# Optimization experiments

Hardware: AMD Instinct MI355X
Metric: run time of the kernel (lower is better)

The kernel has to match this reference:

```python
import jax, jax.numpy as jnp
import numpy as np

B, N, C, H = 2, 2048, 768, 12
DH = C // H
SCALE = DH ** (-0.5)


def setup_inputs() -> dict:
    key = jax.random.key(0)
    k1, k2, k3, k4 = jax.random.split(key, 4)
    x = jax.random.normal(k1, (B, N, 1, C), dtype=jnp.float32)
    mask = jax.random.randint(k2, (B, N), 0, 2) > 0  # bool keep-mask
    w_qkv = jax.random.normal(k3, (3 * C, C), dtype=jnp.float32) * (C ** -0.5)
    w_proj = jax.random.normal(k4, (C, C), dtype=jnp.float32) * (C ** -0.5)
    b_proj = jnp.zeros((C,), dtype=jnp.float32)
    return {"x": x, "mask": mask, "w_qkv": w_qkv, "w_proj": w_proj, "b_proj": b_proj}


def reference(x, mask, w_qkv, w_proj, b_proj):
    Bs, N1, N2, Cs = x.shape  # N2 == 1 required by the original reshape
    # qkv: Linear(dim, 3*dim, bias=False) -> reshape (B,N1,3,H,Dh) -> (3,B,H,N1,Dh)
    qkv = jnp.einsum('bnoc,dc->bnod', x, w_qkv)  # (B,N1,1,3C)
    qkv = qkv.reshape(Bs, N1, 3, H, Cs // H).transpose(2, 0, 3, 1, 4)
    q, k, v = qkv[0], qkv[1], qkv[2]  # each (B,H,N,Dh)
    attn = jnp.einsum('bhid,bhjd->bhij', q, k) * SCALE  # (B,H,N,N)
    mask_value = -jnp.finfo(attn.dtype).max
    pair = mask[:, None, :] & mask[:, :, None]  # (B,N,N), broadcast over heads
    attn = jnp.where(pair[:, None, :, :], attn, mask_value)
    attn = jax.nn.softmax(attn, axis=-1)
    # dropout in eval mode -> identity
    out = jnp.einsum('bhij,bhjd->bhid', attn, v)  # (B,H,N,Dh)
    out = out.transpose(0, 2, 1, 3).reshape(Bs, N1, Cs)  # (B,N,C)
    out = out @ w_proj.T + b_proj
    return out
```

## Files before the change

kernel.cpp:

```cpp
#include <hip/hip_runtime.h>

#define NN 2048
#define CC 768
#define HH 12
#define SCALE2 0.18033688011112042f
#define NEGB  -3.0e35f

typedef __attribute__((ext_vector_type(4))) float f32x4;
typedef __attribute__((ext_vector_type(8))) short short8;
typedef __attribute__((ext_vector_type(8))) unsigned short u16x8;

#if __has_builtin(__builtin_amdgcn_exp2f)
#define EXP2(x) __builtin_amdgcn_exp2f(x)
#else
#define EXP2(x) exp2f(x)
#endif

static __device__ __forceinline__ unsigned short f2bf(float f) {
    unsigned u = __float_as_uint(f);
    u += 0x7FFFu + ((u >> 16) & 1u);
    return (unsigned short)(u >> 16);
}

static __device__ __forceinline__ f32x4 MFMA(u16x8 a, u16x8 b, f32x4 c) {
    union { u16x8 u; short8 s; } ua, ub;
    ua.u = a; ub.u = b;
    return __builtin_amdgcn_mfma_f32_16x16x32_bf16(ua.s, ub.s, c, 0, 0, 0);
}

static __device__ __forceinline__ void glds16(const void* g, void* l) {
    __builtin_amdgcn_global_load_lds(
        (const __attribute__((address_space(1))) unsigned int*)g,
        (__attribute__((address_space(3))) unsigned int*)l, 16, 0, 0);
}

__global__ void cvt_f32_bf16(const float* __restrict__ in,
                             unsigned short* __restrict__ out, int n8) {
    int i = blockIdx.x * blockDim.x + threadIdx.x;
    if (i >= n8) return;
    const f32x4* p = (const f32x4*)(in + (size_t)i * 8);
    f32x4 a = p[0], b = p[1];
    u16x8 o;
    o[0] = f2bf(a[0]); o[1] = f2bf(a[1]); o[2] = f2bf(a[2]); o[3] = f2bf(a[3]);
    o[4] = f2bf(b[0]); o[5] = f2bf(b[1]); o[6] = f2bf(b[2]); o[7] = f2bf(b[3]);
    *(u16x8*)(out + (size_t)i * 8) = o;
}

__launch_bounds__(256)
__global__ void gemm_bt(const unsigned short* __restrict__ A,
                        const unsigned short* __restrict__ Bt,
                        unsigned short* __restrict__ outB,
                        float* __restrict__ outF,
                        const float* __restrict__ bias,
                        int M, int N, int K, int qcols) {
    __shared__ __align__(16) unsigned short As[128][64];
    __shared__ __align__(16) unsigned short Bs[128][64];
    int tid = threadIdx.x, lane = tid & 63, w = tid >> 6;
    int wm = w >> 1, wn = w & 1;
    int li = lane & 15, g = lane >> 4;
    int bn = blockIdx.x, bm = blockIdx.y;

    f32x4 acc[4][4] = {};

    int lrow = lane >> 3, lsl = lane & 7;
    int xcol = (lsl ^ (lrow & 7)) * 8;
    const unsigned short* Ag = A  + (size_t)(bm * 128 + w * 32 + lrow) * K + xcol;
    const unsigned short* Bg = Bt + (size_t)(bn * 128 + w * 32 + lrow) * K + xcol;

    for (int k0 = 0; k0 < K; k0 += 64) {
        __syncthreads();
#pragma unroll
        for (int i = 0; i < 4; ++i) {
            glds16(Ag + (size_t)(i * 8) * K + k0, &As[w * 32 + i * 8][0]);
            glds16(Bg + (size_t)(i * 8) * K + k0, &Bs[w * 32 + i * 8][0]);
        }
        __syncthreads();
#pragma unroll
        for (int kk = 0; kk < 2; ++kk) {
            u16x8 af[4], bf[4];
#pragma unroll
            for (int mi = 0; mi < 4; ++mi)
                af[mi] = *(const u16x8*)&As[wm * 64 + mi * 16 + li][((4 * kk + g) ^ (li & 7)) * 8];
#pragma unroll
            for (int ni = 0; ni < 4; ++ni)
                bf[ni] = *(const u16x8*)&Bs[wn * 64 + ni * 16 + li][((4 * kk + g) ^ (li & 7)) * 8];
            __builtin_amdgcn_s_setprio(1);
#pragma unroll
            for (int mi = 0; mi < 4; ++mi)
#pragma unroll
                for (int ni = 0; ni < 4; ++ni)
                    acc[mi][ni] = MFMA(af[mi], bf[ni], acc[mi][ni]);
            __builtin_amdgcn_s_setprio(0);
        }
    }

#pragma unroll
    for (int mi = 0; mi < 4; ++mi) {
#pragma unroll
        for (int ni = 0; ni < 4; ++ni) {
#pragma unroll
            for (int r = 0; r < 4; ++r) {
                int row = bm * 128 + wm * 64 + mi * 16 + g * 4 + r;
                int col = bn * 128 + wn * 64 + ni * 16 + li;
                float v = acc[mi][ni][r];
                if (outB) {
                    if (col < qcols) v *= SCALE2;
                    outB[(size_t)row * N + col] = f2bf(v);
                } else {
                    outF[(size_t)row * N + col] = v + bias[col];
                }
            }
        }
    }
}

__launch_bounds__(256, 3)
__global__ void attn_kernel(const unsigned short* __restrict__ qkv,
                            const int* __restrict__ mask,
                            unsigned short* __restrict__ hout) {
    __shared__ __align__(16) unsigned short Ks[2][64][64];
    __shared__ __align__(16) unsigned int   Vp[2][64][32];
    __shared__ __align__(16) float pen[NN];

    int tid = threadIdx.x;
    int lane = tid & 63;
    int w = tid >> 6;
    int li = lane & 15, g = lane >> 4;

    int lb = (blockIdx.x & 7) * 96 + (blockIdx.x >> 3);
    int qb = lb & 31;
    int bh = lb >> 5;
    int b = bh / HH, head = bh % HH;
    const int* mb = mask + b * NN;

    {
        int i = tid * 8;
        union { int4 v; int a[4]; } m0, m1;
        m0.v = *(const int4*)&mb[i];
        m1.v = *(const int4*)&mb[i + 4];
        f32x4 p0, p1;
#pragma unroll
        for (int r = 0; r < 4; ++r) {
            p0[r] = m0.a[r] ? 0.f : NEGB;
            p1[r] = m1.a[r] ? 0.f : NEGB;
        }
        *(f32x4*)&pen[i] = p0;
        *(f32x4*)&pen[i + 4] = p1;
    }

    const unsigned short* qbase = qkv + (size_t)(b * NN) * 2304;

    int qrow = qb * 64 + w * 16 + li;
    const unsigned short* qp = qbase + (size_t)qrow * 2304 + head * 64;
    u16x8 qf0 = *(const u16x8*)(qp + g * 8);
    u16x8 qf1 = *(const u16x8*)(qp + 32 + g * 8);
    bool rk = mb[qrow] != 0;
    float pm = rk ? 1.0f : 0.0f;
    if (!rk) {
        qf0 = (u16x8)0;
        qf1 = (u16x8)0;
    }

    int xslot = ((lane & 7) ^ ((lane >> 3) & 7)) * 8;
    const unsigned short* kg = qbase + CC + head * 64 + xslot
                               + (size_t)(w * 16 + (lane >> 3)) * 2304;

    int vm = tid >> 3;
    int vkc = (tid & 7) * 8;
    int vcol = (vm & 16) | ((vm & 6) << 1) | ((vm & 8) >> 2) | (vm & 1);
    int vslot = vcol >> 2, vsub = vcol & 3;
    const unsigned short* vg = qbase + 2 * CC + head * 64 + vkc;

    u16x8 va, vb;
    auto stageK = [&](int buf, int kb) {
        glds16(kg + (size_t)kb * 2304,       &Ks[buf][w * 16][0]);
        glds16(kg + (size_t)(kb + 8) * 2304, &Ks[buf][w * 16 + 8][0]);
    };
    auto loadV = [&](int kb) {
        va = *(const u16x8*)(vg + (size_t)(kb + 2 * vm) * 2304);
        vb = *(const u16x8*)(vg + (size_t)(kb + 2 * vm + 1) * 2304);
    };
    auto writeV = [&](int buf) {
        union { u16x8 v; unsigned u[4]; } ua, ub;
        ua.v = va; ub.v = vb;
        unsigned* vp = &Vp[buf][0][0];
#pragma unroll
        for (int e = 0; e < 8; ++e) {
            int dd = (e + (tid & 7)) & 7;
            unsigned dw = __builtin_amdgcn_perm(ub.u[dd >> 1], ua.u[dd >> 1],
                                                (dd & 1) ? 0x07060302u : 0x05040100u);
            int d0 = vkc + dd;
            vp[d0 * 32 + ((vslot ^ (d0 & 7)) << 2) + vsub] = dw;
        }
    };

    stageK(0, 0);
    loadV(0);
    writeV(0);

    float m_st = -1e30f, l_st = 0.f;
    f32x4 acc[4] = {};
    int cur = 0;

    for (int kb = 0; kb < NN; kb += 64) {
        __syncthreads();
        int nx = cur ^ 1;
        bool more = (kb + 64 < NN);
        if (more) { stageK(nx, kb + 64); loadV(kb + 64); }

        f32x4 st[4];
        __builtin_amdgcn_s_setprio(1);
#pragma unroll
        for (int t = 0; t < 4; ++t) {
            const unsigned short* kr = &Ks[cur][t * 16 + li][0];
            u16x8 k0 = *(const u16x8*)(kr + ((g ^ (li & 7)) * 8));
            u16x8 k1 = *(const u16x8*)(kr + (((4 + g) ^ (li & 7)) * 8));
            f32x4 z = {};
            z = MFMA(k0, qf0, z);
            z = MFMA(k1, qf1, z);
            st[t] = z;
        }
        __builtin_amdgcn_s_setprio(0);

        const float* pp = &pen[kb];
        float tmax = -3.0e38f;
#pragma unroll
        for (int t = 0; t < 4; ++t) {
            f32x4 p4 = *(const f32x4*)&pp[t * 16 + g * 4];
            st[t] += p4 * pm;
            tmax = fmaxf(tmax, fmaxf(fmaxf(st[t][0], st[t][1]),
                                     fmaxf(st[t][2], st[t][3])));
        }
        tmax = fmaxf(tmax, __shfl_xor(tmax, 16));
        tmax = fmaxf(tmax, __shfl_xor(tmax, 32));
        if (__any(tmax > m_st)) {
            float mnew = fmaxf(m_st, tmax);
            float alpha = EXP2(m_st - mnew);
            float ar[4];
#pragma unroll
            for (int r = 0; r < 4; ++r) ar[r] = __shfl(alpha, g * 4 + r);
#pragma unroll
            for (int dt = 0; dt < 4; ++dt)
#pragma unroll
                for (int r = 0; r < 4; ++r) acc[dt][r] *= ar[r];
            l_st *= alpha;
            m_st = mnew;
        }
        float lsum = 0.f;
        union { unsigned u[8]; u16x8 v[2]; } pu;
#pragma unroll
        for (int t = 0; t < 4; ++t) {
            f32x4 e4;
#pragma unroll
            for (int r = 0; r < 4; ++r) { e4[r] = EXP2(st[t][r] - m_st); lsum += e4[r]; }
            pu.u[t * 2]     = __builtin_amdgcn_perm(__float_as_uint(e4[1]),
                                                    __float_as_uint(e4[0]), 0x07060302u);
            pu.u[t * 2 + 1] = __builtin_amdgcn_perm(__float_as_uint(e4[3]),
                                                    __float_as_uint(e4[2]), 0x07060302u);
        }
        lsum += __shfl_xor(lsum, 16);
        lsum += __shfl_xor(lsum, 32);
        l_st += lsum;

        __builtin_amdgcn_s_setprio(1);
#pragma unroll
        for (int h = 0; h < 2; ++h) {
#pragma unroll
            for (int dt = 0; dt < 4; ++dt) {
                const unsigned* vr = &Vp[cur][dt * 16 + li][0];
                u16x8 vf = *(const u16x8*)(vr + (((4 * h + g) ^ (li & 7)) << 2));
                acc[dt] = MFMA(pu.v[h], vf, acc[dt]);
            }
        }
        __builtin_amdgcn_s_setprio(0);

        if (more) writeV(nx);
        cur = nx;
    }

    float linv = 1.0f / l_st;
    float lr[4];
#pragma unroll
    for (int r = 0; r < 4; ++r) lr[r] = __shfl(linv, g * 4 + r);
    size_t obase = ((size_t)(b * NN + qb * 64 + w * 16)) * CC + head * 64;
#pragma unroll
    for (int dt = 0; dt < 4; ++dt) {
#pragma unroll
        for (int r = 0; r < 4; ++r) {
            hout[obase + (size_t)(g * 4 + r) * CC + dt * 16 + li] =
                f2bf(acc[dt][r] * lr[r]);
        }
    }
}

extern "C" void kernel_launch(void* const* d_in, const int* in_sizes, int n_in,
                              void* d_out, int out_size, void* d_ws, size_t ws_size,
                              hipStream_t stream) {
    const float* x     = (const float*)d_in[0];
    const int*   mask  = (const int*)d_in[1];
    const float* wqkv  = (const float*)d_in[2];
    const float* wproj = (const float*)d_in[3];
    const float* bproj = (const float*)d_in[4];
    float* out = (float*)d_out;

    unsigned short* x_bf     = (unsigned short*)d_ws;
    unsigned short* wqkv_bf  = x_bf + 3145728;
    unsigned short* wproj_bf = wqkv_bf + 1769472;
    unsigned short* qkv_bf   = wproj_bf + 589824;
    unsigned short* h_bf     = qkv_bf + 9437184;

    cvt_f32_bf16<<<1536, 256, 0, stream>>>(x, x_bf, 393216);
    cvt_f32_bf16<<<864, 256, 0, stream>>>(wqkv, wqkv_bf, 221184);
    cvt_f32_bf16<<<288, 256, 0, stream>>>(wproj, wproj_bf, 73728);

    gemm_bt<<<dim3(18, 32), 256, 0, stream>>>(x_bf, wqkv_bf, qkv_bf, nullptr,
                                              nullptr, 4096, 2304, 768, 768);
    attn_kernel<<<768, 256, 0, stream>>>(qkv_bf, mask, h_bf);
    gemm_bt<<<dim3(6, 32), 256, 0, stream>>>(h_bf, wproj_bf, nullptr, out,
                                             bproj, 4096, 768, 768, 0);
}
```

Measured before the change: 231.2 us.

## Process two query tiles per wave in attention, halve block threads

The attention kernel now runs 128 threads (2 waves) per block, and each wave handles 32 query rows as two 16-row tiles, so every K and V fragment read from LDS feeds two MFMAs. The V global load is issued two iterations ahead and written to LDS at the start of the next iteration, which deepens prefetch. A lazy rescale threshold (THR=12) skips the online-softmax max update unless the new max exceeds the running max by more than 12 in the log2 domain. These changes cut LDS traffic and rescale work per row, at the cost of higher register pressure and fewer waves per block to hide latency. The threshold also lets exp2 values grow up to 2^12 before bf16 packing, which could slightly affect accuracy.

```diff
diff --git a/kernel.cpp b/kernel.cpp
--- a/kernel.cpp
+++ b/kernel.cpp
@@ -5,6 +5,7 @@
 #define HH 12
 #define SCALE2 0.18033688011112042f
 #define NEGB  -3.0e35f
+#define THR   12.0f
 
 typedef __attribute__((ext_vector_type(4))) float f32x4;
 typedef __attribute__((ext_vector_type(8))) short short8;
@@ -114,7 +115,7 @@
     }
 }
 
-__launch_bounds__(256, 3)
+__launch_bounds__(128, 2)
 __global__ void attn_kernel(const unsigned short* __restrict__ qkv,
                             const int* __restrict__ mask,
                             unsigned short* __restrict__ hout) {
@@ -134,162 +135,183 @@
     const int* mb = mask + b * NN;
 
     {
-        int i = tid * 8;
-        union { int4 v; int a[4]; } m0, m1;
-        m0.v = *(const int4*)&mb[i];
-        m1.v = *(const int4*)&mb[i + 4];
-        f32x4 p0, p1;
-#pragma unroll
-        for (int r = 0; r < 4; ++r) {
-            p0[r] = m0.a[r] ? 0.f : NEGB;
-            p1[r] = m1.a[r] ? 0.f : NEGB;
-        }
-        *(f32x4*)&pen[i] = p0;
-        *(f32x4*)&pen[i + 4] = p1;
+        int i = tid * 16;
+#pragma unroll
+        for (int s = 0; s < 4; ++s) {
+            union { int4 v; int a[4]; } m4;
+            m4.v = *(const int4*)&mb[i + s * 4];
+            f32x4 p;
+#pragma unroll
+            for (int r = 0; r < 4; ++r) p[r] = m4.a[r] ? 0.f : NEGB;
+            *(f32x4*)&pen[i + s * 4] = p;
+        }
     }
 
     const unsigned short* qbase = qkv + (size_t)(b * NN) * 2304;
 
-    int qrow = qb * 64 + w * 16 + li;
-    const unsigned short* qp = qbase + (size_t)qrow * 2304 + head * 64;
-    u16x8 qf0 = *(const u16x8*)(qp + g * 8);
-    u16x8 qf1 = *(const u16x8*)(qp + 32 + g * 8);
-    bool rk = mb[qrow] != 0;
-    float pm = rk ? 1.0f : 0.0f;
-    if (!rk) {
-        qf0 = (u16x8)0;
-        qf1 = (u16x8)0;
+    u16x8 qf[2][2];
+    float pm[2];
+#pragma unroll
+    for (int qt = 0; qt < 2; ++qt) {
+        int qrow = qb * 64 + w * 32 + qt * 16 + li;
+        const unsigned short* qp = qbase + (size_t)qrow * 2304 + head * 64;
+        u16x8 a0 = *(const u16x8*)(qp + g * 8);
+        u16x8 a1 = *(const u16x8*)(qp + 32 + g * 8);
+        bool rk = mb[qrow] != 0;
+        pm[qt] = rk ? 1.f : 0.f;
+        if (!rk) { a0 = (u16x8)0; a1 = (u16x8)0; }
+        qf[qt][0] = a0; qf[qt][1] = a1;
     }
 
     int xslot = ((lane & 7) ^ ((lane >> 3) & 7)) * 8;
     const unsigned short* kg = qbase + CC + head * 64 + xslot
-                               + (size_t)(w * 16 + (lane >> 3)) * 2304;
-
-    int vm = tid >> 3;
+                               + (size_t)(w * 32 + (lane >> 3)) * 2304;
+
+    int m2 = tid >> 3;
     int vkc = (tid & 7) * 8;
-    int vcol = (vm & 16) | ((vm & 6) << 1) | ((vm & 8) >> 2) | (vm & 1);
-    int vslot = vcol >> 2, vsub = vcol & 3;
+    int ma = m2 * 2, mbp = ma + 1;
+    int vca = (ma & 16) | ((ma & 6) << 1) | ((ma & 8) >> 2) | (ma & 1);
+    int vcb = (mbp & 16) | ((mbp & 6) << 1) | ((mbp & 8) >> 2) | (mbp & 1);
     const unsigned short* vg = qbase + 2 * CC + head * 64 + vkc;
 
-    u16x8 va, vb;
+    u16x8 vr0, vr1, vr2, vr3;
     auto stageK = [&](int buf, int kb) {
-        glds16(kg + (size_t)kb * 2304,       &Ks[buf][w * 16][0]);
-        glds16(kg + (size_t)(kb + 8) * 2304, &Ks[buf][w * 16 + 8][0]);
+#pragma unroll
+        for (int s = 0; s < 4; ++s)
+            glds16(kg + (size_t)(kb + s * 8) * 2304, &Ks[buf][w * 32 + s * 8][0]);
     };
     auto loadV = [&](int kb) {
-        va = *(const u16x8*)(vg + (size_t)(kb + 2 * vm) * 2304);
-        vb = *(const u16x8*)(vg + (size_t)(kb + 2 * vm + 1) * 2304);
+        vr0 = *(const u16x8*)(vg + (size_t)(kb + 4 * m2) * 2304);
+        vr1 = *(const u16x8*)(vg + (size_t)(kb + 4 * m2 + 1) * 2304);
+        vr2 = *(const u16x8*)(vg + (size_t)(kb + 4 * m2 + 2) * 2304);
+        vr3 = *(const u16x8*)(vg + (size_t)(kb + 4 * m2 + 3) * 2304);
     };
     auto writeV = [&](int buf) {
-        union { u16x8 v; unsigned u[4]; } ua, ub;
-        ua.v = va; ub.v = vb;
+        union { u16x8 v; unsigned u[4]; } a0, a1, a2, a3;
+        a0.v = vr0; a1.v = vr1; a2.v = vr2; a3.v = vr3;
         unsigned* vp = &Vp[buf][0][0];
 #pragma unroll
         for (int e = 0; e < 8; ++e) {
             int dd = (e + (tid & 7)) & 7;
-            unsigned dw = __builtin_amdgcn_perm(ub.u[dd >> 1], ua.u[dd >> 1],
-                                                (dd & 1) ? 0x07060302u : 0x05040100u);
             int d0 = vkc + dd;
-            vp[d0 * 32 + ((vslot ^ (d0 & 7)) << 2) + vsub] = dw;
+            unsigned dwa = __builtin_amdgcn_perm(a1.u[dd >> 1], a0.u[dd >> 1],
+                                                 (dd & 1) ? 0x07060302u : 0x05040100u);
+            unsigned dwb = __builtin_amdgcn_perm(a3.u[dd >> 1], a2.u[dd >> 1],
+                                                 (dd & 1) ? 0x07060302u : 0x05040100u);
+            vp[d0 * 32 + (((vca >> 2) ^ (d0 & 7)) << 2) + (vca & 3)] = dwa;
+            vp[d0 * 32 + (((vcb >> 2) ^ (d0 & 7)) << 2) + (vcb & 3)] = dwb;
         }
     };
 
     stageK(0, 0);
     loadV(0);
     writeV(0);
-
-    float m_st = -1e30f, l_st = 0.f;
-    f32x4 acc[4] = {};
-    int cur = 0;
-
-    for (int kb = 0; kb < NN; kb += 64) {
+    loadV(64);
+
+    float m_st[2] = {-1e30f, -1e30f};
+    float l_st[2] = {0.f, 0.f};
+    f32x4 acc[2][4] = {};
+
+    for (int it = 0; it < 32; ++it) {
         __syncthreads();
-        int nx = cur ^ 1;
-        bool more = (kb + 64 < NN);
-        if (more) { stageK(nx, kb + 64); loadV(kb + 64); }
-
-        f32x4 st[4];
+        int cur = it & 1, nx = cur ^ 1;
+        if (it < 31) { writeV(nx); stageK(nx, (it + 1) * 64); }
+        if (it < 30) loadV((it + 2) * 64);
+
+        f32x4 st[2][4];
         __builtin_amdgcn_s_setprio(1);
 #pragma unroll
         for (int t = 0; t < 4; ++t) {
             const unsigned short* kr = &Ks[cur][t * 16 + li][0];
             u16x8 k0 = *(const u16x8*)(kr + ((g ^ (li & 7)) * 8));
             u16x8 k1 = *(const u16x8*)(kr + (((4 + g) ^ (li & 7)) * 8));
-            f32x4 z = {};
-            z = MFMA(k0, qf0, z);
-            z = MFMA(k1, qf1, z);
-            st[t] = z;
+            f32x4 z0 = {}, z1 = {};
+            z0 = MFMA(k0, qf[0][0], z0);
+            z1 = MFMA(k0, qf[1][0], z1);
+            z0 = MFMA(k1, qf[0][1], z0);
+            z1 = MFMA(k1, qf[1][1], z1);
+            st[0][t] = z0; st[1][t] = z1;
         }
         __builtin_amdgcn_s_setprio(0);
 
-        const float* pp = &pen[kb];
-        float tmax = -3.0e38f;
-#pragma unroll
-        for (int t = 0; t < 4; ++t) {
-            f32x4 p4 = *(const f32x4*)&pp[t * 16 + g * 4];
-            st[t] += p4 * pm;
-            tmax = fmaxf(tmax, fmaxf(fmaxf(st[t][0], st[t][1]),
-                                     fmaxf(st[t][2], st[t][3])));
-        }
-        tmax = fmaxf(tmax, __shfl_xor(tmax, 16));
-        tmax = fmaxf(tmax, __shfl_xor(tmax, 32));
-        if (__any(tmax > m_st)) {
-            float mnew = fmaxf(m_st, tmax);
-            float alpha = EXP2(m_st - mnew);
-            float ar[4];
-#pragma unroll
-            for (int r = 0; r < 4; ++r) ar[r] = __shfl(alpha, g * 4 + r);
-#pragma unroll
-            for (int dt = 0; dt < 4; ++dt)
-#pragma unroll
-                for (int r = 0; r < 4; ++r) acc[dt][r] *= ar[r];
-            l_st *= alpha;
-            m_st = mnew;
-        }
-        float lsum = 0.f;
-        union { unsigned u[8]; u16x8 v[2]; } pu;
-#pragma unroll
-        for (int t = 0; t < 4; ++t) {
-            f32x4 e4;
-#pragma unroll
-            for (int r = 0; r < 4; ++r) { e4[r] = EXP2(st[t][r] - m_st); lsum += e4[r]; }
-            pu.u[t * 2]     = __builtin_amdgcn_perm(__float_as_uint(e4[1]),
-                                                    __float_as_uint(e4[0]), 0x07060302u);
-            pu.u[t * 2 + 1] = __builtin_amdgcn_perm(__float_as_uint(e4[3]),
-                                                    __float_as_uint(e4[2]), 0x07060302u);
-        }
-        lsum += __shfl_xor(lsum, 16);
-        lsum += __shfl_xor(lsum, 32);
-        l_st += lsum;
+        const float* pp = &pen[it * 64];
+        f32x4 p4[4];
+#pragma unroll
+        for (int t = 0; t < 4; ++t) p4[t] = *(const f32x4*)&pp[t * 16 + g * 4];
+        float lmax[2] = {-3e38f, -3e38f};
+#pragma unroll
+        for (int qt = 0; qt < 2; ++qt)
+#pragma unroll
+            for (int t = 0; t < 4; ++t) {
+                st[qt][t] += p4[t] * pm[qt];
+                lmax[qt] = fmaxf(lmax[qt], fmaxf(fmaxf(st[qt][t][0], st[qt][t][1]),
+                                                 fmaxf(st[qt][t][2], st[qt][t][3])));
+            }
+        bool trig = (lmax[0] > m_st[0] + THR) || (lmax[1] > m_st[1] + THR);
+        if (__any(trig)) {
+#pragma unroll
+            for (int qt = 0; qt < 2; ++qt) {
+                float tm = lmax[qt];
+                tm = fmaxf(tm, __shfl_xor(tm, 16));
+                tm = fmaxf(tm, __shfl_xor(tm, 32));
+                float mnew = fmaxf(m_st[qt], tm);
+                float alpha = EXP2(m_st[qt] - mnew);
+                float ar[4];
+#pragma unroll
+                for (int r = 0; r < 4; ++r) ar[r] = __shfl(alpha, g * 4 + r);
+#pragma unroll
+                for (int dt = 0; dt < 4; ++dt)
+#pragma unroll
+                    for (int r = 0; r < 4; ++r) acc[qt][dt][r] *= ar[r];
+                l_st[qt] *= alpha;
+                m_st[qt] = mnew;
+            }
+        }
+        union { unsigned u[8]; u16x8 v[2]; } pu[2];
+#pragma unroll
+        for (int qt = 0; qt < 2; ++qt) {
+            float lsum = 0.f;
+#pragma unroll
+            for (int t = 0; t < 4; ++t) {
+                f32x4 e4;
+#pragma unroll
+                for (int r = 0; r < 4; ++r) { e4[r] = EXP2(st[qt][t][r] - m_st[qt]); lsum += e4[r]; }
+                pu[qt].u[t * 2]     = __builtin_amdgcn_perm(__float_as_uint(e4[1]),
+                                                            __float_as_uint(e4[0]), 0x07060302u);
+                pu[qt].u[t * 2 + 1] = __builtin_amdgcn_perm(__float_as_uint(e4[3]),
+                                                            __float_as_uint(e4[2]), 0x07060302u);
+            }
+            lsum += __shfl_xor(lsum, 16);
+            lsum += __shfl_xor(lsum, 32);
+            l_st[qt] += lsum;
+        }
 
         __builtin_amdgcn_s_setprio(1);
 #pragma unroll
-        for (int h = 0; h < 2; ++h) {
+        for (int h = 0; h < 2; ++h)
 #pragma unroll
             for (int dt = 0; dt < 4; ++dt) {
                 const unsigned* vr = &Vp[cur][dt * 16 + li][0];
                 u16x8 vf = *(const u16x8*)(vr + (((4 * h + g) ^ (li & 7)) << 2));
-                acc[dt] = MFMA(pu.v[h], vf, acc[dt]);
-            }
-        }
+                acc[0][dt] = MFMA(pu[0].v[h], vf, acc[0][dt]);
+                acc[1][dt] = MFMA(pu[1].v[h], vf, acc[1][dt]);
+            }
         __builtin_amdgcn_s_setprio(0);
-
-        if (more) writeV(nx);
-        cur = nx;
-    }
-
-    float linv = 1.0f / l_st;
-    float lr[4];
-#pragma unroll
-    for (int r = 0; r < 4; ++r) lr[r] = __shfl(linv, g * 4 + r);
-    size_t obase = ((size_t)(b * NN + qb * 64 + w * 16)) * CC + head * 64;
-#pragma unroll
-    for (int dt = 0; dt < 4; ++dt) {
-#pragma unroll
-        for (int r = 0; r < 4; ++r) {
-            hout[obase + (size_t)(g * 4 + r) * CC + dt * 16 + li] =
-                f2bf(acc[dt][r] * lr[r]);
-        }
+    }
+
+#pragma unroll
+    for (int qt = 0; qt < 2; ++qt) {
+        float linv = 1.0f / l_st[qt];
+        float lr[4];
+#pragma unroll
+        for (int r = 0; r < 4; ++r) lr[r] = __shfl(linv, g * 4 + r);
+        size_t obase = ((size_t)(b * NN + qb * 64 + w * 32 + qt * 16)) * CC + head * 64;
+#pragma unroll
+        for (int dt = 0; dt < 4; ++dt)
+#pragma unroll
+            for (int r = 0; r < 4; ++r)
+                hout[obase + (size_t)(g * 4 + r) * CC + dt * 16 + li] =
+                    f2bf(acc[qt][dt][r] * lr[r]);
     }
 }
 
@@ -315,7 +337,7 @@
 
     gemm_bt<<<dim3(18, 32), 256, 0, stream>>>(x_bf, wqkv_bf, qkv_bf, nullptr,
                                               nullptr, 4096, 2304, 768, 768);
-    attn_kernel<<<768, 256, 0, stream>>>(qkv_bf, mask, h_bf);
+    attn_kernel<<<768, 128, 0, stream>>>(qkv_bf, mask, h_bf);
     gemm_bt<<<dim3(6, 32), 256, 0, stream>>>(h_bf, wproj_bf, nullptr, out,
                                              bproj, 4096, 768, 768, 0);
 }
```

Measured after the change: 238.9 us. 1.03x slower.

## Load K directly to registers, widen KV tile to 128, lazy softmax rescale

Applied to the files above, without the earlier changes.

The attention kernel stops staging K through LDS and has each lane read its K fragments straight from global memory into registers. The KV tile per iteration grows from 64 to 128, with V double-buffered in LDS and prefetched two tiles ahead. The online-softmax rescale now fires only when the new max exceeds the running max by a threshold, skipping most rescales. The aim is fewer barriers and less LDS traffic per key, at the cost of uncoalesced, redundant K global loads, more register pressure, and larger exp2 arguments before the max catches up.

```diff
diff --git a/kernel.cpp b/kernel.cpp
--- a/kernel.cpp
+++ b/kernel.cpp
@@ -5,6 +5,7 @@
 #define HH 12
 #define SCALE2 0.18033688011112042f
 #define NEGB  -3.0e35f
+#define THR   12.0f
 
 typedef __attribute__((ext_vector_type(4))) float f32x4;
 typedef __attribute__((ext_vector_type(8))) short short8;
@@ -118,8 +119,7 @@
 __global__ void attn_kernel(const unsigned short* __restrict__ qkv,
                             const int* __restrict__ mask,
                             unsigned short* __restrict__ hout) {
-    __shared__ __align__(16) unsigned short Ks[2][64][64];
-    __shared__ __align__(16) unsigned int   Vp[2][64][32];
+    __shared__ __align__(16) unsigned int Vp[2][2][64][32];
     __shared__ __align__(16) float pen[NN];
 
     int tid = threadIdx.x;
@@ -155,86 +155,91 @@
     u16x8 qf0 = *(const u16x8*)(qp + g * 8);
     u16x8 qf1 = *(const u16x8*)(qp + 32 + g * 8);
     bool rk = mb[qrow] != 0;
-    float pm = rk ? 1.0f : 0.0f;
-    if (!rk) {
-        qf0 = (u16x8)0;
-        qf1 = (u16x8)0;
-    }
-
-    int xslot = ((lane & 7) ^ ((lane >> 3) & 7)) * 8;
-    const unsigned short* kg = qbase + CC + head * 64 + xslot
-                               + (size_t)(w * 16 + (lane >> 3)) * 2304;
-
-    int vm = tid >> 3;
+    float pm = rk ? 1.f : 0.f;
+    if (!rk) { qf0 = (u16x8)0; qf1 = (u16x8)0; }
+
+    const unsigned short* kp = qbase + CC + head * 64 + (size_t)li * 2304 + g * 8;
+
+    int a4 = tid >> 3;
     int vkc = (tid & 7) * 8;
-    int vcol = (vm & 16) | ((vm & 6) << 1) | ((vm & 8) >> 2) | (vm & 1);
-    int vslot = vcol >> 2, vsub = vcol & 3;
+    int sub = a4 >> 4;
+    int jp0 = (2 * a4) & 31, jp1 = jp0 + 1;
+    int vca = (jp0 & 16) | ((jp0 & 6) << 1) | ((jp0 & 8) >> 2) | (jp0 & 1);
+    int vcb = (jp1 & 16) | ((jp1 & 6) << 1) | ((jp1 & 8) >> 2) | (jp1 & 1);
     const unsigned short* vg = qbase + 2 * CC + head * 64 + vkc;
 
-    u16x8 va, vb;
-    auto stageK = [&](int buf, int kb) {
-        glds16(kg + (size_t)kb * 2304,       &Ks[buf][w * 16][0]);
-        glds16(kg + (size_t)(kb + 8) * 2304, &Ks[buf][w * 16 + 8][0]);
-    };
+    u16x8 vr0, vr1, vr2, vr3;
     auto loadV = [&](int kb) {
-        va = *(const u16x8*)(vg + (size_t)(kb + 2 * vm) * 2304);
-        vb = *(const u16x8*)(vg + (size_t)(kb + 2 * vm + 1) * 2304);
+        const unsigned short* p = vg + (size_t)(kb + 4 * a4) * 2304;
+        vr0 = *(const u16x8*)(p);
+        vr1 = *(const u16x8*)(p + 2304);
+        vr2 = *(const u16x8*)(p + 2 * 2304);
+        vr3 = *(const u16x8*)(p + 3 * 2304);
     };
     auto writeV = [&](int buf) {
-        union { u16x8 v; unsigned u[4]; } ua, ub;
-        ua.v = va; ub.v = vb;
-        unsigned* vp = &Vp[buf][0][0];
+        union { u16x8 v; unsigned u[4]; } a0, a1, a2, a3;
+        a0.v = vr0; a1.v = vr1; a2.v = vr2; a3.v = vr3;
+        unsigned* vp = &Vp[buf][sub][0][0];
 #pragma unroll
         for (int e = 0; e < 8; ++e) {
             int dd = (e + (tid & 7)) & 7;
-            unsigned dw = __builtin_amdgcn_perm(ub.u[dd >> 1], ua.u[dd >> 1],
-                                                (dd & 1) ? 0x07060302u : 0x05040100u);
             int d0 = vkc + dd;
-            vp[d0 * 32 + ((vslot ^ (d0 & 7)) << 2) + vsub] = dw;
+            unsigned dwa = __builtin_amdgcn_perm(a1.u[dd >> 1], a0.u[dd >> 1],
+                                                 (dd & 1) ? 0x07060302u : 0x05040100u);
+            unsigned dwb = __builtin_amdgcn_perm(a3.u[dd >> 1], a2.u[dd >> 1],
+                                                 (dd & 1) ? 0x07060302u : 0x05040100u);
+            vp[d0 * 32 + (((vca >> 2) ^ (d0 & 7)) << 2) + (vca & 3)] = dwa;
+            vp[d0 * 32 + (((vcb >> 2) ^ (d0 & 7)) << 2) + (vcb & 3)] = dwb;
         }
     };
 
-    stageK(0, 0);
     loadV(0);
     writeV(0);
+    loadV(128);
 
     float m_st = -1e30f, l_st = 0.f;
     f32x4 acc[4] = {};
-    int cur = 0;
-
-    for (int kb = 0; kb < NN; kb += 64) {
+
+    for (int it = 0; it < 16; ++it) {
         __syncthreads();
-        int nx = cur ^ 1;
-        bool more = (kb + 64 < NN);
-        if (more) { stageK(nx, kb + 64); loadV(kb + 64); }
-
-        f32x4 st[4];
+        int cur = it & 1, nx = cur ^ 1;
+        int kb = it * 128;
+        if (it < 15) writeV(nx);
+        if (it < 14) loadV(kb + 256);
+
+        u16x8 kf[8][2];
+#pragma unroll
+        for (int t = 0; t < 8; ++t) {
+            const unsigned short* kr = kp + (size_t)(kb + t * 16) * 2304;
+            kf[t][0] = *(const u16x8*)(kr);
+            kf[t][1] = *(const u16x8*)(kr + 32);
+        }
+
+        f32x4 st[8];
         __builtin_amdgcn_s_setprio(1);
 #pragma unroll
-        for (int t = 0; t < 4; ++t) {
-            const unsigned short* kr = &Ks[cur][t * 16 + li][0];
-            u16x8 k0 = *(const u16x8*)(kr + ((g ^ (li & 7)) * 8));
-            u16x8 k1 = *(const u16x8*)(kr + (((4 + g) ^ (li & 7)) * 8));
+        for (int t = 0; t < 8; ++t) {
             f32x4 z = {};
-            z = MFMA(k0, qf0, z);
-            z = MFMA(k1, qf1, z);
+            z = MFMA(kf[t][0], qf0, z);
+            z = MFMA(kf[t][1], qf1, z);
             st[t] = z;
         }
         __builtin_amdgcn_s_setprio(0);
 
         const float* pp = &pen[kb];
-        float tmax = -3.0e38f;
-#pragma unroll
-        for (int t = 0; t < 4; ++t) {
+        float lmax = -3e38f;
+#pragma unroll
+        for (int t = 0; t < 8; ++t) {
             f32x4 p4 = *(const f32x4*)&pp[t * 16 + g * 4];
             st[t] += p4 * pm;
-            tmax = fmaxf(tmax, fmaxf(fmaxf(st[t][0], st[t][1]),
+            lmax = fmaxf(lmax, fmaxf(fmaxf(st[t][0], st[t][1]),
                                      fmaxf(st[t][2], st[t][3])));
         }
-        tmax = fmaxf(tmax, __shfl_xor(tmax, 16));
-        tmax = fmaxf(tmax, __shfl_xor(tmax, 32));
-        if (__any(tmax > m_st)) {
-            float mnew = fmaxf(m_st, tmax);
+        if (__any(lmax > m_st + THR)) {
+            float tm = lmax;
+            tm = fmaxf(tm, __shfl_xor(tm, 16));
+            tm = fmaxf(tm, __shfl_xor(tm, 32));
+            float mnew = fmaxf(m_st, tm);
             float alpha = EXP2(m_st - mnew);
             float ar[4];
 #pragma unroll
@@ -247,35 +252,38 @@
             m_st = mnew;
         }
         float lsum = 0.f;
-        union { unsigned u[8]; u16x8 v[2]; } pu;
-#pragma unroll
-        for (int t = 0; t < 4; ++t) {
-            f32x4 e4;
-#pragma unroll
-            for (int r = 0; r < 4; ++r) { e4[r] = EXP2(st[t][r] - m_st); lsum += e4[r]; }
-            pu.u[t * 2]     = __builtin_amdgcn_perm(__float_as_uint(e4[1]),
-                                                    __float_as_uint(e4[0]), 0x07060302u);
-            pu.u[t * 2 + 1] = __builtin_amdgcn_perm(__float_as_uint(e4[3]),
-                                                    __float_as_uint(e4[2]), 0x07060302u);
-        }
+        union { unsigned u[8]; u16x8 v[2]; } pu[2];
+#pragma unroll
+        for (int s = 0; s < 2; ++s)
+#pragma unroll
+            for (int t = 0; t < 4; ++t) {
+                f32x4 e4;
+#pragma unroll
+                for (int r = 0; r < 4; ++r) {
+                    e4[r] = EXP2(st[s * 4 + t][r] - m_st);
+                    lsum += e4[r];
+                }
+                pu[s].u[t * 2]     = __builtin_amdgcn_perm(__float_as_uint(e4[1]),
+                                                           __float_as_uint(e4[0]), 0x07060302u);
+                pu[s].u[t * 2 + 1] = __builtin_amdgcn_perm(__float_as_uint(e4[3]),
+                                                           __float_as_uint(e4[2]), 0x07060302u);
+            }
         lsum += __shfl_xor(lsum, 16);
         lsum += __shfl_xor(lsum, 32);
         l_st += lsum;
 
         __builtin_amdgcn_s_setprio(1);
 #pragma unroll
-        for (int h = 0; h < 2; ++h) {
-#pragma unroll
-            for (int dt = 0; dt < 4; ++dt) {
-                const unsigned* vr = &Vp[cur][dt * 16 + li][0];
-                u16x8 vf = *(const u16x8*)(vr + (((4 * h + g) ^ (li & 7)) << 2));
-                acc[dt] = MFMA(pu.v[h], vf, acc[dt]);
-            }
-        }
+        for (int s = 0; s < 2; ++s)
+#pragma unroll
+            for (int h = 0; h < 2; ++h)
+#pragma unroll
+                for (int dt = 0; dt < 4; ++dt) {
+                    const unsigned* vr = &Vp[cur][s][dt * 16 + li][0];
+                    u16x8 vf = *(const u16x8*)(vr + (((4 * h + g) ^ (li & 7)) << 2));
+                    acc[dt] = MFMA(pu[s].v[h], vf, acc[dt]);
+                }
         __builtin_amdgcn_s_setprio(0);
-
-        if (more) writeV(nx);
-        cur = nx;
     }
 
     float linv = 1.0f / l_st;
@@ -284,13 +292,11 @@
     for (int r = 0; r < 4; ++r) lr[r] = __shfl(linv, g * 4 + r);
     size_t obase = ((size_t)(b * NN + qb * 64 + w * 16)) * CC + head * 64;
 #pragma unroll
-    for (int dt = 0; dt < 4; ++dt) {
-#pragma unroll
-        for (int r = 0; r < 4; ++r) {
+    for (int dt = 0; dt < 4; ++dt)
+#pragma unroll
+        for (int r = 0; r < 4; ++r)
             hout[obase + (size_t)(g * 4 + r) * CC + dt * 16 + li] =
                 f2bf(acc[dt][r] * lr[r]);
-        }
-    }
 }
 
 extern "C" void kernel_launch(void* const* d_in, const int* in_sizes, int n_in,
```

Measured after the change: 294.1 us. 1.27x slower.

## Prefetch V two tiles ahead, lazy softmax rescale, defer row-sum reduction

Applied to the files above, without the earlier changes.

Restructures the flash-attention loop. V global loads now run two iterations ahead, with the LDS write placed at the top of each iteration so it no longer sits after the PV MFMAs. The mask penalty is loaded as the MFMA accumulator init. The running max is only updated when a lane's local max exceeds it by a threshold (12 in log2 units), which skips most rescale work and cross-lane max shuffles. Row-sum shuffles move out of the loop to a single reduction at the end. This adds register pressure and lets exponentials grow up to 2^12 before bf16 conversion, which trades some numeric headroom.

```diff
diff --git a/kernel.cpp b/kernel.cpp
--- a/kernel.cpp
+++ b/kernel.cpp
@@ -5,6 +5,7 @@
 #define HH 12
 #define SCALE2 0.18033688011112042f
 #define NEGB  -3.0e35f
+#define THR   12.0f
 
 typedef __attribute__((ext_vector_type(4))) float f32x4;
 typedef __attribute__((ext_vector_type(8))) short short8;
@@ -155,11 +156,8 @@
     u16x8 qf0 = *(const u16x8*)(qp + g * 8);
     u16x8 qf1 = *(const u16x8*)(qp + 32 + g * 8);
     bool rk = mb[qrow] != 0;
-    float pm = rk ? 1.0f : 0.0f;
-    if (!rk) {
-        qf0 = (u16x8)0;
-        qf1 = (u16x8)0;
-    }
+    float pm = rk ? 1.f : 0.f;
+    if (!rk) { qf0 = (u16x8)0; qf1 = (u16x8)0; }
 
     int xslot = ((lane & 7) ^ ((lane >> 3) & 7)) * 8;
     const unsigned short* kg = qbase + CC + head * 64 + xslot
@@ -197,16 +195,23 @@
     stageK(0, 0);
     loadV(0);
     writeV(0);
-
-    float m_st = -1e30f, l_st = 0.f;
+    loadV(64);
+
+    float m_st = -1e30f;
+    float l_part = 0.f;
     f32x4 acc[4] = {};
-    int cur = 0;
-
-    for (int kb = 0; kb < NN; kb += 64) {
+
+    for (int it = 0; it < 32; ++it) {
         __syncthreads();
-        int nx = cur ^ 1;
-        bool more = (kb + 64 < NN);
-        if (more) { stageK(nx, kb + 64); loadV(kb + 64); }
+        int cur = it & 1, nx = cur ^ 1;
+        if (it < 31) { writeV(nx); stageK(nx, (it + 1) * 64); }
+        if (it < 30) loadV((it + 2) * 64);
+
+        const float* pp = &pen[it * 64];
+        f32x4 ci[4];
+#pragma unroll
+        for (int t = 0; t < 4; ++t)
+            ci[t] = (*(const f32x4*)&pp[t * 16 + g * 4]) * pm;
 
         f32x4 st[4];
         __builtin_amdgcn_s_setprio(1);
@@ -215,26 +220,23 @@
             const unsigned short* kr = &Ks[cur][t * 16 + li][0];
             u16x8 k0 = *(const u16x8*)(kr + ((g ^ (li & 7)) * 8));
             u16x8 k1 = *(const u16x8*)(kr + (((4 + g) ^ (li & 7)) * 8));
-            f32x4 z = {};
+            f32x4 z = ci[t];
             z = MFMA(k0, qf0, z);
             z = MFMA(k1, qf1, z);
             st[t] = z;
         }
         __builtin_amdgcn_s_setprio(0);
 
-        const float* pp = &pen[kb];
-        float tmax = -3.0e38f;
-#pragma unroll
-        for (int t = 0; t < 4; ++t) {
-            f32x4 p4 = *(const f32x4*)&pp[t * 16 + g * 4];
-            st[t] += p4 * pm;
-            tmax = fmaxf(tmax, fmaxf(fmaxf(st[t][0], st[t][1]),
+        float lmax = -3e38f;
+#pragma unroll
+        for (int t = 0; t < 4; ++t)
+            lmax = fmaxf(lmax, fmaxf(fmaxf(st[t][0], st[t][1]),
                                      fmaxf(st[t][2], st[t][3])));
-        }
-        tmax = fmaxf(tmax, __shfl_xor(tmax, 16));
-        tmax = fmaxf(tmax, __shfl_xor(tmax, 32));
-        if (__any(tmax > m_st)) {
-            float mnew = fmaxf(m_st, tmax);
+        if (__any(lmax > m_st + THR)) {
+            float tm = lmax;
+            tm = fmaxf(tm, __shfl_xor(tm, 16));
+            tm = fmaxf(tm, __shfl_xor(tm, 32));
+            float mnew = fmaxf(m_st, tm);
             float alpha = EXP2(m_st - mnew);
             float ar[4];
 #pragma unroll
@@ -243,54 +245,47 @@
             for (int dt = 0; dt < 4; ++dt)
 #pragma unroll
                 for (int r = 0; r < 4; ++r) acc[dt][r] *= ar[r];
-            l_st *= alpha;
+            l_part *= alpha;
             m_st = mnew;
         }
-        float lsum = 0.f;
         union { unsigned u[8]; u16x8 v[2]; } pu;
 #pragma unroll
         for (int t = 0; t < 4; ++t) {
             f32x4 e4;
 #pragma unroll
-            for (int r = 0; r < 4; ++r) { e4[r] = EXP2(st[t][r] - m_st); lsum += e4[r]; }
+            for (int r = 0; r < 4; ++r) { e4[r] = EXP2(st[t][r] - m_st); l_part += e4[r]; }
             pu.u[t * 2]     = __builtin_amdgcn_perm(__float_as_uint(e4[1]),
                                                     __float_as_uint(e4[0]), 0x07060302u);
             pu.u[t * 2 + 1] = __builtin_amdgcn_perm(__float_as_uint(e4[3]),
                                                     __float_as_uint(e4[2]), 0x07060302u);
         }
-        lsum += __shfl_xor(lsum, 16);
-        lsum += __shfl_xor(lsum, 32);
-        l_st += lsum;
 
         __builtin_amdgcn_s_setprio(1);
 #pragma unroll
-        for (int h = 0; h < 2; ++h) {
+        for (int h = 0; h < 2; ++h)
 #pragma unroll
             for (int dt = 0; dt < 4; ++dt) {
                 const unsigned* vr = &Vp[cur][dt * 16 + li][0];
                 u16x8 vf = *(const u16x8*)(vr + (((4 * h + g) ^ (li & 7)) << 2));
                 acc[dt] = MFMA(pu.v[h], vf, acc[dt]);
             }
-        }
         __builtin_amdgcn_s_setprio(0);
-
-        if (more) writeV(nx);
-        cur = nx;
     }
 
+    float l_st = l_part;
+    l_st += __shfl_xor(l_st, 16);
+    l_st += __shfl_xor(l_st, 32);
     float linv = 1.0f / l_st;
     float lr[4];
 #pragma unroll
     for (int r = 0; r < 4; ++r) lr[r] = __shfl(linv, g * 4 + r);
     size_t obase = ((size_t)(b * NN + qb * 64 + w * 16)) * CC + head * 64;
 #pragma unroll
-    for (int dt = 0; dt < 4; ++dt) {
-#pragma unroll
-        for (int r = 0; r < 4; ++r) {
+    for (int dt = 0; dt < 4; ++dt)
+#pragma unroll
+        for (int r = 0; r < 4; ++r)
             hout[obase + (size_t)(g * 4 + r) * CC + dt * 16 + li] =
                 f2bf(acc[dt][r] * lr[r]);
-        }
-    }
 }
 
 extern "C" void kernel_launch(void* const* d_in, const int* in_sizes, int n_in,
```

After: 224.1 us. -3.1%, faster.
